# Optimization experiments

Measured on AMD Instinct MI355X. Metric: run time of the kernel, lower is better.

The kernel has to match this reference:

```python
import jax, jax.numpy as jnp
import numpy as np

N_NODES = 100000
N_EDGES = 1000000
NEG_SLOPE = 0.2


def gat_conv(x, src, dst, W, al, ar, b, res, activation):
    """DGL-style GATConv. res is None (no residual), 'id' (identity residual), or a [in,H*D] matrix."""
    H, D = al.shape
    n = x.shape[0]
    feat = (x @ W).reshape(n, H, D)                      # [N,H,D]
    el = jnp.einsum('nhd,hd->nh', feat, al)              # [N,H]
    er = jnp.einsum('nhd,hd->nh', feat, ar)              # [N,H]
    e = jax.nn.leaky_relu(el[src] + er[dst], NEG_SLOPE)  # [E,H]
    # edge softmax over incoming edges of each dst node
    m = jax.lax.stop_gradient(jax.ops.segment_max(e, dst, num_segments=n))
    ex = jnp.exp(e - m[dst])
    s = jax.ops.segment_sum(ex, dst, num_segments=n)
    alpha = ex / s[dst]                                  # [E,H]
    out = jax.ops.segment_sum(feat[src] * alpha[:, :, None], dst, num_segments=n)  # [N,H,D]
    if res == 'id':
        out = out + x.reshape(n, H, D)
    elif res is not None:
        out = out + (x @ res).reshape(n, H, D)
    out = out + b.reshape(1, H, D)
    if activation is not None:
        out = activation(out)
    return out


def setup_inputs() -> dict:
    key = jax.random.key(0)
    ks = jax.random.split(key, 20)
    F_IN, HID = 128, 32
    H1, H2, H3 = 4, 4, 1
    C = 40
    sc = 0.1
    inp = {
        'x':   jax.random.normal(ks[0], (N_NODES, F_IN), dtype=jnp.float32),
        'src': jax.random.randint(ks[1], (N_EDGES,), 0, N_NODES, dtype=jnp.int32),
        'dst': jax.random.randint(ks[2], (N_EDGES,), 0, N_NODES, dtype=jnp.int32),
        # layer 1: in=128 -> H1*HID=128, no residual, elu
        'W1':  sc * jax.random.normal(ks[3], (F_IN, H1 * HID), dtype=jnp.float32),
        'al1': sc * jax.random.normal(ks[4], (H1, HID), dtype=jnp.float32),
        'ar1': sc * jax.random.normal(ks[5], (H1, HID), dtype=jnp.float32),
        'b1':  jnp.zeros((H1 * HID,), dtype=jnp.float32),
        # layer 2: in=128 -> H2*HID=128, identity residual, elu
        'W2':  sc * jax.random.normal(ks[6], (H1 * HID, H2 * HID), dtype=jnp.float32),
        'al2': sc * jax.random.normal(ks[7], (H2, HID), dtype=jnp.float32),
        'ar2': sc * jax.random.normal(ks[8], (H2, HID), dtype=jnp.float32),
        'b2':  jnp.zeros((H2 * HID,), dtype=jnp.float32),
        # layer 3 (output): in=128 -> H3*HID=32, projected residual, no activation
        'W3':  sc * jax.random.normal(ks[9], (H2 * HID, H3 * HID), dtype=jnp.float32),
        'al3': sc * jax.random.normal(ks[10], (H3, HID), dtype=jnp.float32),
        'ar3': sc * jax.random.normal(ks[11], (H3, HID), dtype=jnp.float32),
        'b3':  jnp.zeros((H3 * HID,), dtype=jnp.float32),
        'res3': sc * jax.random.normal(ks[12], (H2 * HID, H3 * HID), dtype=jnp.float32),
        # final classifier
        'Wfc': sc * jax.random.normal(ks[13], (HID, C), dtype=jnp.float32),
        'bfc': jnp.zeros((C,), dtype=jnp.float32),
    }
    return inp


def reference(x, src, dst, W1, al1, ar1, b1, W2, al2, ar2, b2, W3, al3, ar3, b3, res3, Wfc, bfc):
    n = x.shape[0]
    h = gat_conv(x, src, dst, W1, al1, ar1, b1, None, jax.nn.elu).reshape(n, -1)   # [N, 128]
    h = gat_conv(h, src, dst, W2, al2, ar2, b2, 'id', jax.nn.elu).reshape(n, -1)   # [N, 128]
    h = gat_conv(h, src, dst, W3, al3, ar3, b3, res3, None).mean(axis=1)           # [N, 32]
    return h @ Wfc + bfc                                                           # [N, 40]
```

## Files before the change

### kernel.cpp

```cpp
#include <hip/hip_runtime.h>
#include <cstdint>
#include <cstddef>

#define NN 100000
#define NE 1000000
#define GEMM_BLOCKS 1563
#define TICKET_BLOCKS 3907
#define CAST_BLOCKS 12500
#define LOG2E 1.4426950408896340736f

typedef unsigned int uint;
typedef unsigned short ushort;
typedef __attribute__((ext_vector_type(8))) short bfrag;
typedef __attribute__((ext_vector_type(4))) float f32x4;

__device__ __forceinline__ ushort f2bf(float f){
  uint u = __float_as_uint(f);
  u += 0x7fffu + ((u >> 16) & 1u);
  return (ushort)(u >> 16);
}
__device__ __forceinline__ float bflo(uint p){ return __uint_as_float(p << 16); }
__device__ __forceinline__ float bfhi(uint p){ return __uint_as_float(p & 0xffff0000u); }


__global__ __launch_bounds__(256) void k_scan_local(const int* __restrict__ cnt, int* __restrict__ rowptr,
                                                    int* __restrict__ bsum){
  __shared__ int sm[256];
  int t = threadIdx.x;
  int i = blockIdx.x*256 + t;
  int v = (i < NN) ? cnt[i] : 0;
  sm[t] = v;
  __syncthreads();
  for (int off=1; off<256; off<<=1){
    int u = (t>=off) ? sm[t-off] : 0;
    __syncthreads();
    sm[t] += u;
    __syncthreads();
  }
  if (i < NN) rowptr[i] = sm[t] - v;
  if (t == 255) bsum[blockIdx.x] = sm[255];
}

__global__ __launch_bounds__(512) void k_scan_bsum(const int* __restrict__ bsum, int* __restrict__ boff, int nb){
  __shared__ int sm[512];
  int t = threadIdx.x;
  int v = (t < nb) ? bsum[t] : 0;
  sm[t] = v;
  __syncthreads();
  for (int off=1; off<512; off<<=1){
    int u = (t>=off) ? sm[t-off] : 0;
    __syncthreads();
    sm[t] += u;
    __syncthreads();
  }
  if (t < nb) boff[t] = sm[t] - v;
}

__global__ __launch_bounds__(256) void k_scan_add(int* __restrict__ rowptr, const int* __restrict__ boff){
  int i = blockIdx.x*256 + threadIdx.x;
  if (i < NN) rowptr[i] += boff[i>>8];
  else if (i == NN) rowptr[NN] = NE;
}


__device__ __forceinline__ void bfrag_body(const float* __restrict__ B1, const float* __restrict__ B2,
                                           int n1, int n2, int NT, ushort* __restrict__ out, int i){
  if (i >= NT*4*64) return;
  int l = i & 63, ks = (i>>6)&3, nt = i>>8;
  int col = nt*16 + (l&15);
  int k0  = ks*32 + (l>>4)*8;
  const float* B; int stride, c;
  if (col < n1){ B = B1; stride = n1; c = col; }
  else         { B = B2; stride = n2; c = col - n1; }
  ushort v[8];
  #pragma unroll
  for (int j=0;j<8;j++) v[j] = f2bf(B[(size_t)(k0+j)*stride + c]);
  uint4 pk;
  pk.x = (uint)v[0] | ((uint)v[1]<<16);
  pk.y = (uint)v[2] | ((uint)v[3]<<16);
  pk.z = (uint)v[4] | ((uint)v[5]<<16);
  pk.w = (uint)v[6] | ((uint)v[7]<<16);
  *(uint4*)(out + (size_t)i*8) = pk;
}

__global__ __launch_bounds__(256) void k_prep(const float* __restrict__ x, ushort* __restrict__ xb,
                                              const float* __restrict__ W1, const float* __restrict__ W2,
                                              const float* __restrict__ W3, const float* __restrict__ res3,
                                              ushort* __restrict__ Bf1, ushort* __restrict__ Bf2,
                                              ushort* __restrict__ Bf3,
                                              const int* __restrict__ dst, int* __restrict__ cnt,
                                              int* __restrict__ tick){
  int bid = blockIdx.x, t = threadIdx.x;
  if (bid < CAST_BLOCKS){
    int i = bid*256 + t;
    float4 v = ((const float4*)x)[i];
    uint2 p;
    p.x = (uint)f2bf(v.x) | ((uint)f2bf(v.y)<<16);
    p.y = (uint)f2bf(v.z) | ((uint)f2bf(v.w)<<16);
    ((uint2*)xb)[i] = p;
  } else if (bid < CAST_BLOCKS + 20){
    int r = bid - CAST_BLOCKS;
    if (r < 8)       bfrag_body(W1, nullptr, 128, 0, 8, Bf1, r*256 + t);
    else if (r < 16) bfrag_body(W2, nullptr, 128, 0, 8, Bf2, (r-8)*256 + t);
    else             bfrag_body(W3, res3,    32, 32, 4, Bf3, (r-16)*256 + t);
  } else {
    int e = (bid - CAST_BLOCKS - 20)*256 + t;
    if (e < NE) tick[e] = atomicAdd(&cnt[dst[e]], 1);
  }
}


template<int NT, int NTF, int H>
__device__ __forceinline__ void gemm_body(int bid, const ushort* __restrict__ Ab, const ushort* __restrict__ Bf,
                                          ushort* __restrict__ featb, float* __restrict__ Cres,
                                          const float* __restrict__ al, const float* __restrict__ ar,
                                          float* __restrict__ el, float* __restrict__ er, int M){
  int t = threadIdx.x;
  int l = t & 63, w = t >> 6;
  int rw = bid*64 + w*16;
  int c = l & 15, g = l >> 4;

  f32x4 acc[NT];
  #pragma unroll
  for (int nt=0;nt<NT;nt++) acc[nt] = (f32x4){0.f,0.f,0.f,0.f};

  int rowA = rw + c; if (rowA >= M) rowA = M-1;
  const ushort* Ap = Ab + (size_t)rowA*128 + g*8;
  const bfrag* Bp = (const bfrag*)Bf;

  #pragma unroll
  for (int ks=0; ks<4; ++ks){
    bfrag a = *(const bfrag*)(Ap + ks*32);
    #pragma unroll
    for (int nt=0; nt<NT; ++nt){
      bfrag b = Bp[(nt*4+ks)*64 + l];
      acc[nt] = __builtin_amdgcn_mfma_f32_16x16x32_bf16(a, b, acc[nt], 0, 0, 0);
    }
  }

  float alv[H][2], arv[H][2];
  #pragma unroll
  for (int h=0;h<H;h++){
    alv[h][0]=al[h*32+c]*LOG2E;    arv[h][0]=ar[h*32+c]*LOG2E;
    alv[h][1]=al[h*32+16+c]*LOG2E; arv[h][1]=ar[h*32+16+c]*LOG2E;
  }

  #pragma unroll
  for (int reg=0; reg<4; ++reg){
    int row = rw + g*4 + reg;
    bool ok = row < M;
    #pragma unroll
    for (int h=0;h<H;h++){
      float pl = acc[2*h][reg]*alv[h][0] + acc[2*h+1][reg]*alv[h][1];
      float pr = acc[2*h][reg]*arv[h][0] + acc[2*h+1][reg]*arv[h][1];
      #pragma unroll
      for (int off=1; off<16; off<<=1){ pl += __shfl_xor(pl,off); pr += __shfl_xor(pr,off); }
      if (ok && c==0){ el[(size_t)row*H + h] = pl; er[(size_t)row*H + h] = pr; }
    }
    if (ok){
      #pragma unroll
      for (int nt=0; nt<NTF; ++nt)
        featb[(size_t)row*(NTF*16) + nt*16 + c] = f2bf(acc[nt][reg]);
      #pragma unroll
      for (int nt=NTF; nt<NT; ++nt)
        Cres[(size_t)row*((NT-NTF)*16) + (nt-NTF)*16 + c] = acc[nt][reg];
    }
  }
}

template<int NT, int NTF, int H>
__global__ __launch_bounds__(256) void k_gemm_mfma(const ushort* __restrict__ Ab, const ushort* __restrict__ Bf,
                                                   ushort* __restrict__ featb, float* __restrict__ Cres,
                                                   const float* __restrict__ al, const float* __restrict__ ar,
                                                   float* __restrict__ el, float* __restrict__ er, int M){
  gemm_body<NT,NTF,H>(blockIdx.x, Ab, Bf, featb, Cres, al, ar, el, er, M);
}

__global__ __launch_bounds__(256) void k_gemm1_place(const ushort* __restrict__ xb, const ushort* __restrict__ Bf1,
                                                     ushort* __restrict__ featb,
                                                     const float* __restrict__ al, const float* __restrict__ ar,
                                                     float* __restrict__ el, float* __restrict__ er,
                                                     const int* __restrict__ src, const int* __restrict__ dst,
                                                     const int* __restrict__ rowptr, const int* __restrict__ tick,
                                                     int* __restrict__ csr){
  int bid = blockIdx.x;
  if (bid < GEMM_BLOCKS){
    gemm_body<8,8,4>(bid, xb, Bf1, featb, nullptr, al, ar, el, er, NN);
  } else {
    int e = (bid - GEMM_BLOCKS)*256 + threadIdx.x;
    if (e < NE){
      int d = dst[e];
      csr[rowptr[d] + tick[e]] = src[e];
    }
  }
}


template<int RK>
__global__ __launch_bounds__(256) void k_agg4(const int* __restrict__ rowptr, const int* __restrict__ csr,
                                              const ushort* __restrict__ feat,
                                              const float* __restrict__ el, const float* __restrict__ er,
                                              const void* __restrict__ res, const float* __restrict__ bias,
                                              ushort* __restrict__ out, int act){
  int lane = threadIdx.x & 63;
  int node = blockIdx.x*4 + (threadIdx.x >> 6);

  int beg = rowptr[node], deg = rowptr[node+1] - beg;
  int q = lane >> 4, l15 = lane & 15;
  int hm = l15 >> 2;
  float erh = er[(size_t)node*4 + hm];
  const int* cp = csr + beg;
  uint fo = (uint)l15*8u;

  float ssum = 0.f;
  float a0=0.f,a1=0.f,a2=0.f,a3=0.f,a4=0.f,a5=0.f,a6=0.f,a7=0.f;

  int ei = q;
  for (; ei + 4 < deg; ei += 8){
    int s0 = cp[ei], s1 = cp[ei+4];
    uint4 p0 = *(const uint4*)(feat + ((uint)s0*128u + fo));
    uint4 p1 = *(const uint4*)(feat + ((uint)s1*128u + fo));
    float v0 = el[(uint)s0*4u + hm] + erh; v0 = fmaxf(v0, 0.2f*v0);
    float v1 = el[(uint)s1*4u + hm] + erh; v1 = fmaxf(v1, 0.2f*v1);
    float w0 = __builtin_amdgcn_exp2f(v0);
    float w1 = __builtin_amdgcn_exp2f(v1);
    ssum += w0 + w1;
    a0 += w0*bflo(p0.x) + w1*bflo(p1.x);
    a1 += w0*bfhi(p0.x) + w1*bfhi(p1.x);
    a2 += w0*bflo(p0.y) + w1*bflo(p1.y);
    a3 += w0*bfhi(p0.y) + w1*bfhi(p1.y);
    a4 += w0*bflo(p0.z) + w1*bflo(p1.z);
    a5 += w0*bfhi(p0.z) + w1*bfhi(p1.z);
    a6 += w0*bflo(p0.w) + w1*bflo(p1.w);
    a7 += w0*bfhi(p0.w) + w1*bfhi(p1.w);
  }
  if (ei < deg){
    int s0 = cp[ei];
    uint4 p0 = *(const uint4*)(feat + ((uint)s0*128u + fo));
    float v0 = el[(uint)s0*4u + hm] + erh; v0 = fmaxf(v0, 0.2f*v0);
    float w0 = __builtin_amdgcn_exp2f(v0);
    ssum += w0;
    a0 += w0*bflo(p0.x); a1 += w0*bfhi(p0.x);
    a2 += w0*bflo(p0.y); a3 += w0*bfhi(p0.y);
    a4 += w0*bflo(p0.z); a5 += w0*bfhi(p0.z);
    a6 += w0*bflo(p0.w); a7 += w0*bfhi(p0.w);
  }

  #pragma unroll
  for (int off=16; off<64; off<<=1){
    ssum += __shfl_xor(ssum, off);
    a0 += __shfl_xor(a0, off); a1 += __shfl_xor(a1, off);
    a2 += __shfl_xor(a2, off); a3 += __shfl_xor(a3, off);
    a4 += __shfl_xor(a4, off); a5 += __shfl_xor(a5, off);
    a6 += __shfl_xor(a6, off); a7 += __shfl_xor(a7, off);
  }
  float inv = (deg > 0) ? 1.f/ssum : 0.f;

  if (lane < 16){
    float o0=a0*inv, o1=a1*inv, o2=a2*inv, o3=a3*inv;
    float o4=a4*inv, o5=a5*inv, o6=a6*inv, o7=a7*inv;
    if (RK == 1){
      uint4 rv = *(const uint4*)((const ushort*)res + (size_t)node*128 + l15*8);
      o0 += bflo(rv.x); o1 += bfhi(rv.x); o2 += bflo(rv.y); o3 += bfhi(rv.y);
      o4 += bflo(rv.z); o5 += bfhi(rv.z); o6 += bflo(rv.w); o7 += bfhi(rv.w);
    }
    float4 bv0 = *(const float4*)(bias + l15*8);
    float4 bv1 = *(const float4*)(bias + l15*8 + 4);
    o0 += bv0.x; o1 += bv0.y; o2 += bv0.z; o3 += bv0.w;
    o4 += bv1.x; o5 += bv1.y; o6 += bv1.z; o7 += bv1.w;
    if (act){
      o0 = (o0>0.f)?o0:__expf(o0)-1.f;
      o1 = (o1>0.f)?o1:__expf(o1)-1.f;
      o2 = (o2>0.f)?o2:__expf(o2)-1.f;
      o3 = (o3>0.f)?o3:__expf(o3)-1.f;
      o4 = (o4>0.f)?o4:__expf(o4)-1.f;
      o5 = (o5>0.f)?o5:__expf(o5)-1.f;
      o6 = (o6>0.f)?o6:__expf(o6)-1.f;
      o7 = (o7>0.f)?o7:__expf(o7)-1.f;
    }
    uint4 pk;
    pk.x = (uint)f2bf(o0) | ((uint)f2bf(o1)<<16);
    pk.y = (uint)f2bf(o2) | ((uint)f2bf(o3)<<16);
    pk.z = (uint)f2bf(o4) | ((uint)f2bf(o5)<<16);
    pk.w = (uint)f2bf(o6) | ((uint)f2bf(o7)<<16);
    *(uint4*)(out + (size_t)node*128 + l15*8) = pk;
  }
}


__global__ __launch_bounds__(256) void k_agg1(const int* __restrict__ rowptr, const int* __restrict__ csr,
                                              const ushort* __restrict__ feat,
                                              const float* __restrict__ el, const float* __restrict__ er,
                                              const float* __restrict__ res, const float* __restrict__ bias,
                                              float* __restrict__ h3){
  int lane = threadIdx.x & 63;
  int node = blockIdx.x*4 + (threadIdx.x >> 6);

  int beg = rowptr[node], deg = rowptr[node+1] - beg;
  int sub = lane >> 3, fl = lane & 7;
  float er0 = er[node];
  const int* cp = csr + beg;
  uint fo = (uint)fl*4u;

  float ssum = 0.f, a0=0.f, a1=0.f, a2=0.f, a3=0.f;
  for (int ei = sub; ei < deg; ei += 8){
    int s = cp[ei];
    uint2 pv = *(const uint2*)(feat + ((uint)s*32u + fo));
    float v = el[s] + er0; v = fmaxf(v, 0.2f*v);
    float w = __builtin_amdgcn_exp2f(v);
    ssum += w;
    a0 += w*bflo(pv.x); a1 += w*bfhi(pv.x);
    a2 += w*bflo(pv.y); a3 += w*bfhi(pv.y);
  }
  #pragma unroll
  for (int off=8; off<64; off<<=1){
    ssum += __shfl_xor(ssum, off);
    a0 += __shfl_xor(a0, off); a1 += __shfl_xor(a1, off);
    a2 += __shfl_xor(a2, off); a3 += __shfl_xor(a3, off);
  }
  float inv = (deg > 0) ? 1.f/ssum : 0.f;

  if (lane < 8){
    float4 rv = *(const float4*)(res + (size_t)node*32 + fl*4);
    float4 bv = *(const float4*)(bias + fl*4);
    float4 ov;
    ov.x = a0*inv + rv.x + bv.x;
    ov.y = a1*inv + rv.y + bv.y;
    ov.z = a2*inv + rv.z + bv.z;
    ov.w = a3*inv + rv.w + bv.w;
    *(float4*)(h3 + (size_t)node*32 + fl*4) = ov;
  }
}


__global__ __launch_bounds__(256) void k_fc(const float* __restrict__ h, const float* __restrict__ W,
                                            const float* __restrict__ b, float* __restrict__ out){
  __shared__ float Ws[32*40];
  __shared__ float Hs[64][33];
  __shared__ float bs[40];
  int t = threadIdx.x;
  for (int i=t; i<1280; i+=256) Ws[i] = W[i];
  if (t < 40) bs[t] = b[t];
  int n0 = blockIdx.x*64;
  for (int idx=t; idx<512; idx+=256){
    int r = idx>>3, c4 = idx&7;
    float4 v;
    if (n0 + r < NN) v = *(const float4*)(h + (size_t)(n0+r)*32 + c4*4);
    else v = make_float4(0.f,0.f,0.f,0.f);
    Hs[r][c4*4+0]=v.x; Hs[r][c4*4+1]=v.y; Hs[r][c4*4+2]=v.z; Hs[r][c4*4+3]=v.w;
  }
  __syncthreads();
  int n = t>>2, cg = t&3;
  float acc[10];
  #pragma unroll
  for (int j=0;j<10;j++) acc[j] = 0.f;
  #pragma unroll
  for (int k=0;k<32;k++){
    float hv = Hs[n][k];
    #pragma unroll
    for (int j=0;j<10;j++) acc[j] += hv * Ws[k*40 + cg + 4*j];
  }
  int row = n0 + n;
  if (row < NN){
    #pragma unroll
    for (int j=0;j<10;j++) out[(size_t)row*40 + cg + 4*j] = acc[j] + bs[cg+4*j];
  }
}


extern "C" void kernel_launch(void* const* d_in, const int* in_sizes, int n_in,
                              void* d_out, int out_size, void* d_ws, size_t ws_size,
                              hipStream_t stream){
  const float* x    = (const float*)d_in[0];
  const int*   src  = (const int*)  d_in[1];
  const int*   dst  = (const int*)  d_in[2];
  const float* W1   = (const float*)d_in[3];
  const float* al1  = (const float*)d_in[4];
  const float* ar1  = (const float*)d_in[5];
  const float* b1   = (const float*)d_in[6];
  const float* W2   = (const float*)d_in[7];
  const float* al2  = (const float*)d_in[8];
  const float* ar2  = (const float*)d_in[9];
  const float* b2   = (const float*)d_in[10];
  const float* W3   = (const float*)d_in[11];
  const float* al3  = (const float*)d_in[12];
  const float* ar3  = (const float*)d_in[13];
  const float* b3   = (const float*)d_in[14];
  const float* res3 = (const float*)d_in[15];
  const float* Wfc  = (const float*)d_in[16];
  const float* bfc  = (const float*)d_in[17];
  float* out = (float*)d_out;

  char* ws = (char*)d_ws;
  size_t o = 0;
  auto alloc = [&](size_t bytes)->char*{
    char* p = ws + o;
    o += (bytes + 255) & ~(size_t)255;
    return p;
  };
  int*    rowptr = (int*)   alloc((size_t)(NN+1)*4);
  int*    cnt    = (int*)   alloc((size_t)NN*4);
  int*    bsum   = (int*)   alloc(512*4);
  int*    boff   = (int*)   alloc(512*4);
  int*    tick   = (int*)   alloc((size_t)NE*4);
  int*    csr    = (int*)   alloc((size_t)NE*4);
  float*  el     = (float*) alloc((size_t)NN*4*4);
  float*  er     = (float*) alloc((size_t)NN*4*4);
  ushort* xb     = (ushort*)alloc((size_t)NN*128*2);
  ushort* featb  = (ushort*)alloc((size_t)NN*128*2);
  ushort* h1b    = (ushort*)alloc((size_t)NN*128*2);
  ushort* h2b    = (ushort*)alloc((size_t)NN*128*2);
  float*  res3p  = (float*) alloc((size_t)NN*32*4);
  float*  h3     = (float*) alloc((size_t)NN*32*4);
  ushort* Bf1    = (ushort*)alloc((size_t)8*4*64*8*2);
  ushort* Bf2    = (ushort*)alloc((size_t)8*4*64*8*2);
  ushort* Bf3    = (ushort*)alloc((size_t)4*4*64*8*2);
  (void)ws_size; (void)n_in; (void)in_sizes; (void)out_size;

  hipMemsetAsync(cnt, 0, (size_t)NN*4, stream);
  k_prep<<<CAST_BLOCKS+20+TICKET_BLOCKS, 256, 0, stream>>>(x, xb, W1, W2, W3, res3,
                                                           Bf1, Bf2, Bf3, dst, cnt, tick);
  int nb = (NN+255)/256;
  k_scan_local<<<nb, 256, 0, stream>>>(cnt, rowptr, bsum);
  k_scan_bsum<<<1, 512, 0, stream>>>(bsum, boff, nb);
  k_scan_add<<<(NN+1+255)/256, 256, 0, stream>>>(rowptr, boff);

  k_gemm1_place<<<GEMM_BLOCKS+TICKET_BLOCKS, 256, 0, stream>>>(xb, Bf1, featb, al1, ar1, el, er,
                                                               src, dst, rowptr, tick, csr);
  k_agg4<0><<<NN/4, 256, 0, stream>>>(rowptr, csr, featb, el, er, nullptr, b1, h1b, 1);

  k_gemm_mfma<8,8,4><<<GEMM_BLOCKS, 256, 0, stream>>>(h1b, Bf2, featb, nullptr, al2, ar2, el, er, NN);
  k_agg4<1><<<NN/4, 256, 0, stream>>>(rowptr, csr, featb, el, er, h1b, b2, h2b, 1);

  k_gemm_mfma<4,2,1><<<GEMM_BLOCKS, 256, 0, stream>>>(h2b, Bf3, featb, res3p, al3, ar3, el, er, NN);
  k_agg1<<<NN/4, 256, 0, stream>>>(rowptr, csr, featb, el, er, res3p, b3, h3);
  k_fc<<<GEMM_BLOCKS, 256, 0, stream>>>(h3, Wfc, bfc, out);
}
```

Before: 294.2 us.

## Sort nodes by degree and assign one sub-wavefront group per node in aggregation

Builds a degree histogram, scans it, and scatters nodes into a degree-sorted permutation so that nodes with similar in-degree share a wavefront. The aggregation kernels switch from one wavefront per node, with edges split across quarters and then reduced by shuffles, to 16 lanes per node (8 for the last layer) that walk all of the node's edges serially. This removes the cross-lane reductions and the idle lanes at the write stage, while the sorting keeps divergence between nodes in a wave low. Separately, the GEMM now stages the B fragments in shared memory. The costs are three extra small kernels with atomics and longer serial edge loops per lane.

Result: slower. 948.3 us (+222.4%).

```diff
diff --git a/kernel.cpp b/kernel.cpp
--- a/kernel.cpp
+++ b/kernel.cpp
@@ -60,6 +60,40 @@
   int i = blockIdx.x*256 + threadIdx.x;
   if (i < NN) rowptr[i] += boff[i>>8];
   else if (i == NN) rowptr[NN] = NE;
+}
+
+
+__global__ __launch_bounds__(256) void k_dhist(const int* __restrict__ rowptr, int* __restrict__ dbin){
+  int n = blockIdx.x*256 + threadIdx.x;
+  if (n < NN){
+    int deg = rowptr[n+1] - rowptr[n];
+    atomicAdd(&dbin[deg > 255 ? 255 : deg], 1);
+  }
+}
+
+__global__ __launch_bounds__(256) void k_dscan(int* __restrict__ dbin){
+  __shared__ int sm[256];
+  int t = threadIdx.x;
+  int v = dbin[t];
+  sm[t] = v;
+  __syncthreads();
+  for (int off=1; off<256; off<<=1){
+    int u = (t>=off) ? sm[t-off] : 0;
+    __syncthreads();
+    sm[t] += u;
+    __syncthreads();
+  }
+  dbin[t] = sm[t] - v;
+}
+
+__global__ __launch_bounds__(256) void k_dscat(const int* __restrict__ rowptr, int* __restrict__ dbin,
+                                               int* __restrict__ perm){
+  int n = blockIdx.x*256 + threadIdx.x;
+  if (n < NN){
+    int deg = rowptr[n+1] - rowptr[n];
+    int p = atomicAdd(&dbin[deg > 255 ? 255 : deg], 1);
+    perm[p] = n;
+  }
 }
 
 
@@ -115,7 +149,13 @@
                                           ushort* __restrict__ featb, float* __restrict__ Cres,
                                           const float* __restrict__ al, const float* __restrict__ ar,
                                           float* __restrict__ el, float* __restrict__ er, int M){
-  int t = threadIdx.x;
+  __shared__ ushort Bs[NT*2048];
+  int t = threadIdx.x;
+  #pragma unroll
+  for (int i=0; i<NT; ++i)
+    ((uint4*)Bs)[i*256 + t] = ((const uint4*)Bf)[i*256 + t];
+  __syncthreads();
+
   int l = t & 63, w = t >> 6;
   int rw = bid*64 + w*16;
   int c = l & 15, g = l >> 4;
@@ -126,7 +166,7 @@
 
   int rowA = rw + c; if (rowA >= M) rowA = M-1;
   const ushort* Ap = Ab + (size_t)rowA*128 + g*8;
-  const bfrag* Bp = (const bfrag*)Bf;
+  const bfrag* Bp = (const bfrag*)Bs;
 
   #pragma unroll
   for (int ks=0; ks<4; ++ks){
@@ -198,15 +238,16 @@
 
 template<int RK>
 __global__ __launch_bounds__(256) void k_agg4(const int* __restrict__ rowptr, const int* __restrict__ csr,
+                                              const int* __restrict__ perm,
                                               const ushort* __restrict__ feat,
                                               const float* __restrict__ el, const float* __restrict__ er,
                                               const void* __restrict__ res, const float* __restrict__ bias,
                                               ushort* __restrict__ out, int act){
-  int lane = threadIdx.x & 63;
-  int node = blockIdx.x*4 + (threadIdx.x >> 6);
+  int t = threadIdx.x;
+  int l15 = t & 15;
+  int node = perm[blockIdx.x*16 + (t>>4)];
 
   int beg = rowptr[node], deg = rowptr[node+1] - beg;
-  int q = lane >> 4, l15 = lane & 15;
   int hm = l15 >> 2;
   float erh = er[(size_t)node*4 + hm];
   const int* cp = csr + beg;
@@ -215,9 +256,9 @@
   float ssum = 0.f;
   float a0=0.f,a1=0.f,a2=0.f,a3=0.f,a4=0.f,a5=0.f,a6=0.f,a7=0.f;
 
-  int ei = q;
-  for (; ei + 4 < deg; ei += 8){
-    int s0 = cp[ei], s1 = cp[ei+4];
+  int ei = 0;
+  for (; ei+2 <= deg; ei += 2){
+    int s0 = cp[ei], s1 = cp[ei+1];
     uint4 p0 = *(const uint4*)(feat + ((uint)s0*128u + fo));
     uint4 p1 = *(const uint4*)(feat + ((uint)s1*128u + fo));
     float v0 = el[(uint)s0*4u + hm] + erh; v0 = fmaxf(v0, 0.2f*v0);
@@ -246,90 +287,87 @@
     a6 += w0*bflo(p0.w); a7 += w0*bfhi(p0.w);
   }
 
-  #pragma unroll
-  for (int off=16; off<64; off<<=1){
-    ssum += __shfl_xor(ssum, off);
-    a0 += __shfl_xor(a0, off); a1 += __shfl_xor(a1, off);
-    a2 += __shfl_xor(a2, off); a3 += __shfl_xor(a3, off);
-    a4 += __shfl_xor(a4, off); a5 += __shfl_xor(a5, off);
-    a6 += __shfl_xor(a6, off); a7 += __shfl_xor(a7, off);
-  }
   float inv = (deg > 0) ? 1.f/ssum : 0.f;
-
-  if (lane < 16){
-    float o0=a0*inv, o1=a1*inv, o2=a2*inv, o3=a3*inv;
-    float o4=a4*inv, o5=a5*inv, o6=a6*inv, o7=a7*inv;
-    if (RK == 1){
-      uint4 rv = *(const uint4*)((const ushort*)res + (size_t)node*128 + l15*8);
-      o0 += bflo(rv.x); o1 += bfhi(rv.x); o2 += bflo(rv.y); o3 += bfhi(rv.y);
-      o4 += bflo(rv.z); o5 += bfhi(rv.z); o6 += bflo(rv.w); o7 += bfhi(rv.w);
-    }
-    float4 bv0 = *(const float4*)(bias + l15*8);
-    float4 bv1 = *(const float4*)(bias + l15*8 + 4);
-    o0 += bv0.x; o1 += bv0.y; o2 += bv0.z; o3 += bv0.w;
-    o4 += bv1.x; o5 += bv1.y; o6 += bv1.z; o7 += bv1.w;
-    if (act){
-      o0 = (o0>0.f)?o0:__expf(o0)-1.f;
-      o1 = (o1>0.f)?o1:__expf(o1)-1.f;
-      o2 = (o2>0.f)?o2:__expf(o2)-1.f;
-      o3 = (o3>0.f)?o3:__expf(o3)-1.f;
-      o4 = (o4>0.f)?o4:__expf(o4)-1.f;
-      o5 = (o5>0.f)?o5:__expf(o5)-1.f;
-      o6 = (o6>0.f)?o6:__expf(o6)-1.f;
-      o7 = (o7>0.f)?o7:__expf(o7)-1.f;
-    }
-    uint4 pk;
-    pk.x = (uint)f2bf(o0) | ((uint)f2bf(o1)<<16);
-    pk.y = (uint)f2bf(o2) | ((uint)f2bf(o3)<<16);
-    pk.z = (uint)f2bf(o4) | ((uint)f2bf(o5)<<16);
-    pk.w = (uint)f2bf(o6) | ((uint)f2bf(o7)<<16);
-    *(uint4*)(out + (size_t)node*128 + l15*8) = pk;
-  }
+  float o0=a0*inv, o1=a1*inv, o2=a2*inv, o3=a3*inv;
+  float o4=a4*inv, o5=a5*inv, o6=a6*inv, o7=a7*inv;
+  if (RK == 1){
+    uint4 rv = *(const uint4*)((const ushort*)res + (size_t)node*128 + fo);
+    o0 += bflo(rv.x); o1 += bfhi(rv.x); o2 += bflo(rv.y); o3 += bfhi(rv.y);
+    o4 += bflo(rv.z); o5 += bfhi(rv.z); o6 += bflo(rv.w); o7 += bfhi(rv.w);
+  }
+  float4 bv0 = *(const float4*)(bias + l15*8);
+  float4 bv1 = *(const float4*)(bias + l15*8 + 4);
+  o0 += bv0.x; o1 += bv0.y; o2 += bv0.z; o3 += bv0.w;
+  o4 += bv1.x; o5 += bv1.y; o6 += bv1.z; o7 += bv1.w;
+  if (act){
+    o0 = (o0>0.f)?o0:__expf(o0)-1.f;
+    o1 = (o1>0.f)?o1:__expf(o1)-1.f;
+    o2 = (o2>0.f)?o2:__expf(o2)-1.f;
+    o3 = (o3>0.f)?o3:__expf(o3)-1.f;
+    o4 = (o4>0.f)?o4:__expf(o4)-1.f;
+    o5 = (o5>0.f)?o5:__expf(o5)-1.f;
+    o6 = (o6>0.f)?o6:__expf(o6)-1.f;
+    o7 = (o7>0.f)?o7:__expf(o7)-1.f;
+  }
+  uint4 pk;
+  pk.x = (uint)f2bf(o0) | ((uint)f2bf(o1)<<16);
+  pk.y = (uint)f2bf(o2) | ((uint)f2bf(o3)<<16);
+  pk.z = (uint)f2bf(o4) | ((uint)f2bf(o5)<<16);
+  pk.w = (uint)f2bf(o6) | ((uint)f2bf(o7)<<16);
+  *(uint4*)(out + (size_t)node*128 + fo) = pk;
 }
 
 
 __global__ __launch_bounds__(256) void k_agg1(const int* __restrict__ rowptr, const int* __restrict__ csr,
+                                              const int* __restrict__ perm,
                                               const ushort* __restrict__ feat,
                                               const float* __restrict__ el, const float* __restrict__ er,
                                               const float* __restrict__ res, const float* __restrict__ bias,
                                               float* __restrict__ h3){
-  int lane = threadIdx.x & 63;
-  int node = blockIdx.x*4 + (threadIdx.x >> 6);
+  int t = threadIdx.x;
+  int l7 = t & 7;
+  int node = perm[blockIdx.x*32 + (t>>3)];
 
   int beg = rowptr[node], deg = rowptr[node+1] - beg;
-  int sub = lane >> 3, fl = lane & 7;
   float er0 = er[node];
   const int* cp = csr + beg;
-  uint fo = (uint)fl*4u;
+  uint fo = (uint)l7*4u;
 
   float ssum = 0.f, a0=0.f, a1=0.f, a2=0.f, a3=0.f;
-  for (int ei = sub; ei < deg; ei += 8){
-    int s = cp[ei];
-    uint2 pv = *(const uint2*)(feat + ((uint)s*32u + fo));
-    float v = el[s] + er0; v = fmaxf(v, 0.2f*v);
-    float w = __builtin_amdgcn_exp2f(v);
-    ssum += w;
-    a0 += w*bflo(pv.x); a1 += w*bfhi(pv.x);
-    a2 += w*bflo(pv.y); a3 += w*bfhi(pv.y);
-  }
-  #pragma unroll
-  for (int off=8; off<64; off<<=1){
-    ssum += __shfl_xor(ssum, off);
-    a0 += __shfl_xor(a0, off); a1 += __shfl_xor(a1, off);
-    a2 += __shfl_xor(a2, off); a3 += __shfl_xor(a3, off);
-  }
+  int ei = 0;
+  for (; ei+2 <= deg; ei += 2){
+    int s0 = cp[ei], s1 = cp[ei+1];
+    uint2 p0 = *(const uint2*)(feat + ((uint)s0*32u + fo));
+    uint2 p1 = *(const uint2*)(feat + ((uint)s1*32u + fo));
+    float v0 = el[s0] + er0; v0 = fmaxf(v0, 0.2f*v0);
+    float v1 = el[s1] + er0; v1 = fmaxf(v1, 0.2f*v1);
+    float w0 = __builtin_amdgcn_exp2f(v0);
+    float w1 = __builtin_amdgcn_exp2f(v1);
+    ssum += w0 + w1;
+    a0 += w0*bflo(p0.x) + w1*bflo(p1.x);
+    a1 += w0*bfhi(p0.x) + w1*bfhi(p1.x);
+    a2 += w0*bflo(p0.y) + w1*bflo(p1.y);
+    a3 += w0*bfhi(p0.y) + w1*bfhi(p1.y);
+  }
+  if (ei < deg){
+    int s0 = cp[ei];
+    uint2 p0 = *(const uint2*)(feat + ((uint)s0*32u + fo));
+    float v0 = el[s0] + er0; v0 = fmaxf(v0, 0.2f*v0);
+    float w0 = __builtin_amdgcn_exp2f(v0);
+    ssum += w0;
+    a0 += w0*bflo(p0.x); a1 += w0*bfhi(p0.x);
+    a2 += w0*bflo(p0.y); a3 += w0*bfhi(p0.y);
+  }
+
   float inv = (deg > 0) ? 1.f/ssum : 0.f;
-
-  if (lane < 8){
-    float4 rv = *(const float4*)(res + (size_t)node*32 + fl*4);
-    float4 bv = *(const float4*)(bias + fl*4);
-    float4 ov;
-    ov.x = a0*inv + rv.x + bv.x;
-    ov.y = a1*inv + rv.y + bv.y;
-    ov.z = a2*inv + rv.z + bv.z;
-    ov.w = a3*inv + rv.w + bv.w;
-    *(float4*)(h3 + (size_t)node*32 + fl*4) = ov;
-  }
+  float4 rv = *(const float4*)(res + (size_t)node*32 + fo);
+  float4 bv = *(const float4*)(bias + fo);
+  float4 ov;
+  ov.x = a0*inv + rv.x + bv.x;
+  ov.y = a1*inv + rv.y + bv.y;
+  ov.z = a2*inv + rv.z + bv.z;
+  ov.w = a3*inv + rv.w + bv.w;
+  *(float4*)(h3 + (size_t)node*32 + fo) = ov;
 }
 
 
@@ -402,6 +440,8 @@
   int*    cnt    = (int*)   alloc((size_t)NN*4);
   int*    bsum   = (int*)   alloc(512*4);
   int*    boff   = (int*)   alloc(512*4);
+  int*    dbin   = (int*)   alloc(256*4);
+  int*    perm   = (int*)   alloc((size_t)NN*4);
   int*    tick   = (int*)   alloc((size_t)NE*4);
   int*    csr    = (int*)   alloc((size_t)NE*4);
   float*  el     = (float*) alloc((size_t)NN*4*4);
@@ -418,6 +458,7 @@
   (void)ws_size; (void)n_in; (void)in_sizes; (void)out_size;
 
   hipMemsetAsync(cnt, 0, (size_t)NN*4, stream);
+  hipMemsetAsync(dbin, 0, 256*4, stream);
   k_prep<<<CAST_BLOCKS+20+TICKET_BLOCKS, 256, 0, stream>>>(x, xb, W1, W2, W3, res3,
                                                            Bf1, Bf2, Bf3, dst, cnt, tick);
   int nb = (NN+255)/256;
@@ -425,14 +466,18 @@
   k_scan_bsum<<<1, 512, 0, stream>>>(bsum, boff, nb);
   k_scan_add<<<(NN+1+255)/256, 256, 0, stream>>>(rowptr, boff);
 
+  k_dhist<<<nb, 256, 0, stream>>>(rowptr, dbin);
+  k_dscan<<<1, 256, 0, stream>>>(dbin);
+  k_dscat<<<nb, 256, 0, stream>>>(rowptr, dbin, perm);
+
   k_gemm1_place<<<GEMM_BLOCKS+TICKET_BLOCKS, 256, 0, stream>>>(xb, Bf1, featb, al1, ar1, el, er,
                                                                src, dst, rowptr, tick, csr);
-  k_agg4<0><<<NN/4, 256, 0, stream>>>(rowptr, csr, featb, el, er, nullptr, b1, h1b, 1);
+  k_agg4<0><<<NN/16, 256, 0, stream>>>(rowptr, csr, perm, featb, el, er, nullptr, b1, h1b, 1);
 
   k_gemm_mfma<8,8,4><<<GEMM_BLOCKS, 256, 0, stream>>>(h1b, Bf2, featb, nullptr, al2, ar2, el, er, NN);
-  k_agg4<1><<<NN/4, 256, 0, stream>>>(rowptr, csr, featb, el, er, h1b, b2, h2b, 1);
+  k_agg4<1><<<NN/16, 256, 0, stream>>>(rowptr, csr, perm, featb, el, er, h1b, b2, h2b, 1);
 
   k_gemm_mfma<4,2,1><<<GEMM_BLOCKS, 256, 0, stream>>>(h2b, Bf3, featb, res3p, al3, ar3, el, er, NN);
-  k_agg1<<<NN/4, 256, 0, stream>>>(rowptr, csr, featb, el, er, res3p, b3, h3);
+  k_agg1<<<NN/32, 256, 0, stream>>>(rowptr, csr, perm, featb, el, er, res3p, b3, h3);
   k_fc<<<GEMM_BLOCKS, 256, 0, stream>>>(h3, Wfc, bfc, out);
 }
```
